# Performance work log

Hardware: AMD Instinct MI355X
Metric: run time of the kernel (lower is better)

Reference implementation:

```python
import jax, jax.numpy as jnp
import numpy as np

GROUP_SIZE = 64
OUT_F, IN_F = 4096, 4096


def _dequantize_3bit(packed_u8, params, group_size):
    # packed_u8: [num_groups * group_size//8*3] uint8; params: [num_groups, 2] (min, max)
    p = packed_u8.reshape(-1, 3)
    b0, b1, b2 = p[:, 0], p[:, 1], p[:, 2]
    q = jnp.stack([
        b0 & 7,
        (b0 >> 3) & 7,
        ((b0 >> 6) & 3) | ((b1 & 1) << 2),
        (b1 >> 1) & 7,
        (b1 >> 4) & 7,
        ((b1 >> 7) & 1) | ((b2 & 3) << 1),
        (b2 >> 2) & 7,
        (b2 >> 5) & 7,
    ], axis=-1)  # [N8, 8] uint8 in [0,7]
    num_groups = params.shape[0]
    q = q.reshape(num_groups, group_size).astype(jnp.float32)
    pf = params.astype(jnp.float32)
    x_min = pf[:, 0:1]
    scale = pf[:, 1:2] - x_min
    w = (q / 7.0) * scale + x_min
    return w.reshape(-1)


def setup_inputs() -> dict:
    key = jax.random.key(0)
    k1, k2, k3, k4 = jax.random.split(key, 4)
    num_groups = OUT_F * IN_F // GROUP_SIZE
    num_packed = num_groups * (GROUP_SIZE // 8 * 3)
    x = jax.random.normal(k1, (4, 2048, IN_F), dtype=jnp.float32)
    weight_q3 = jax.random.randint(k2, (num_packed,), 0, 256, dtype=jnp.int32)
    # realistic params: min < max per group
    raw = jax.random.normal(k3, (num_groups, 2), dtype=jnp.float32) * 0.02
    lo = jnp.minimum(raw[:, 0], raw[:, 1]) - 0.01
    hi = jnp.maximum(raw[:, 0], raw[:, 1]) + 0.01
    weight_params = jnp.stack([lo, hi], axis=-1).astype(jnp.float16)
    bias = jax.random.normal(k4, (OUT_F,), dtype=jnp.float32) * 0.02
    return {"x": x, "weight_q3": weight_q3, "weight_params": weight_params, "bias": bias}


def reference(x, weight_q3, weight_params, bias):
    packed = weight_q3.astype(jnp.uint8)
    w = _dequantize_3bit(packed, weight_params, GROUP_SIZE).reshape(OUT_F, IN_F)
    # F.linear: x @ W^T + b
    return jnp.einsum('bsi,oi->bso', x, w) + bias
```

## Files before the change

kernel.cpp:

```cpp
#include <hip/hip_runtime.h>
#include <hip/hip_fp16.h>
#include <stdint.h>

#define OUT_F 4096
#define IN_F  4096
#define M_DIM 8192
#define K_DIM IN_F
#define N_DIM OUT_F
#define GROUPS (OUT_F * IN_F / 64)
#define NTRIP  (GROUPS * 8)
#define NPARAM (GROUPS * 2)
#define NIT    (K_DIM / 128)

typedef __attribute__((ext_vector_type(4))) float f32x4;
typedef __attribute__((ext_vector_type(8))) short bf16x8;
typedef __attribute__((ext_vector_type(8))) unsigned short u16x8;

static __device__ __forceinline__ unsigned short f32_to_bf16(float f) {
    unsigned int u = __builtin_bit_cast(unsigned int, f);
    u += 0x7fffu + ((u >> 16) & 1u);
    return (unsigned short)(u >> 16);
}

__global__ void flag_init(int* f) { f[0] = 0; }

__global__ __launch_bounds__(256) void detect_f16(const __half* __restrict__ p,
                                                  int* __restrict__ flag) {
    int big = 0;
    for (int i = blockIdx.x * 256 + threadIdx.x; i < NPARAM; i += 256 * 256) {
        float v = __half2float(p[i]);
        if (!(fabsf(v) < 1.0f)) big = 1;
    }
    if (big) atomicOr(flag, 1);
}

__global__ __launch_bounds__(256) void dequant3(const int* __restrict__ pk,
                                                const void* __restrict__ params,
                                                const int* __restrict__ flag,
                                                unsigned short* __restrict__ W) {
    int t = blockIdx.x * 256 + threadIdx.x;
    int b0 = pk[3 * t + 0];
    int b1 = pk[3 * t + 1];
    int b2 = pk[3 * t + 2];
    int g = t >> 3;
    float lo, hi;
    if (flag[0] == 0) {
        const __half* p = (const __half*)params;
        lo = __half2float(p[2 * g + 0]);
        hi = __half2float(p[2 * g + 1]);
    } else {
        const float* p = (const float*)params;
        lo = p[2 * g + 0];
        hi = p[2 * g + 1];
    }
    float s = (hi - lo) * (1.0f / 7.0f);

    int q[8];
    q[0] = b0 & 7;
    q[1] = (b0 >> 3) & 7;
    q[2] = ((b0 >> 6) & 3) | ((b1 & 1) << 2);
    q[3] = (b1 >> 1) & 7;
    q[4] = (b1 >> 4) & 7;
    q[5] = ((b1 >> 7) & 1) | ((b2 & 3) << 1);
    q[6] = (b2 >> 2) & 7;
    q[7] = (b2 >> 5) & 7;

    u16x8 o;
#pragma unroll
    for (int j = 0; j < 8; j++) {
        float w = (float)q[j] * s + lo;
        o[j] = f32_to_bf16(w);
    }
    *(u16x8*)&W[8 * (size_t)t] = o;
}

__global__ __launch_bounds__(256) void cvt_x(const float* __restrict__ x,
                                             unsigned short* __restrict__ xb) {
    size_t t = (size_t)blockIdx.x * 256 + threadIdx.x;
    f32x4 a = *(const f32x4*)&x[8 * t];
    f32x4 b = *(const f32x4*)&x[8 * t + 4];
    u16x8 o;
#pragma unroll
    for (int j = 0; j < 4; j++) o[j] = f32_to_bf16(a[j]);
#pragma unroll
    for (int j = 0; j < 4; j++) o[4 + j] = f32_to_bf16(b[j]);
    *(u16x8*)&xb[8 * t] = o;
}


#define READ_AH(dst, b, h) do { _Pragma("unroll") for (int m2_ = 0; m2_ < 4; ++m2_) { \
    const char* p_ = shb + (b) * 49152 + arow_b + ((h) * 4 + m2_) * 2048; \
    dst[m2_][0] = *(const bf16x8*)(p_ + cb0); \
    dst[m2_][1] = *(const bf16x8*)(p_ + cb1); } } while (0)

#define READ_BT(dst, b) do { _Pragma("unroll") for (int n_ = 0; n_ < 2; ++n_) { \
    const char* p_ = shb + (b) * 49152 + 32768 + brow_b + n_ * 2048; \
    dst[n_][0] = *(const bf16x8*)(p_ + cb0); \
    dst[n_][1] = *(const bf16x8*)(p_ + cb1); } } while (0)

#define MFMA_H(h, As, Bs) do { __builtin_amdgcn_s_setprio(1); \
  _Pragma("unroll") for (int m2_ = 0; m2_ < 4; ++m2_) \
  _Pragma("unroll") for (int n_ = 0; n_ < 2; ++n_) { \
    acc[(h)*4+m2_][n_] = __builtin_amdgcn_mfma_f32_16x16x32_bf16(As[m2_][0], Bs[n_][0], acc[(h)*4+m2_][n_], 0,0,0); \
    acc[(h)*4+m2_][n_] = __builtin_amdgcn_mfma_f32_16x16x32_bf16(As[m2_][1], Bs[n_][1], acc[(h)*4+m2_][n_], 0,0,0); } \
  __builtin_amdgcn_s_setprio(0); } while (0)

#define STAGE_A(b, kt) do { _Pragma("unroll") for (int c_ = 0; c_ < 4; ++c_) { \
    const char* g_ = GAb + (size_t)(kt) * 128 + (size_t)(c_ * 64) * 8192; \
    unsigned short* l_ = &sh[(b) * 24576 + c_ * 4096 + w * 512]; \
    __builtin_amdgcn_global_load_lds((const __attribute__((address_space(1))) unsigned int*)(g_ + voff), \
        (__attribute__((address_space(3))) unsigned int*)l_, 16, 0, 0); } } while (0)

#define STAGE_B(b, kt) do { _Pragma("unroll") for (int c_ = 0; c_ < 2; ++c_) { \
    const char* g_ = GBb + (size_t)(kt) * 128 + (size_t)(c_ * 64) * 8192; \
    unsigned short* l_ = &sh[(b) * 24576 + 16384 + c_ * 4096 + w * 512]; \
    __builtin_amdgcn_global_load_lds((const __attribute__((address_space(1))) unsigned int*)(g_ + voff), \
        (__attribute__((address_space(3))) unsigned int*)l_, 16, 0, 0); } } while (0)

#define BAR() asm volatile("s_barrier" ::: "memory")
#define VMW(n) asm volatile("s_waitcnt vmcnt(" #n ")" ::: "memory")

__global__ __launch_bounds__(512, 1) void gemm4(const unsigned short* __restrict__ A,
                                                const unsigned short* __restrict__ B,
                                                const float* __restrict__ bias,
                                                float* __restrict__ C) {
    __shared__ unsigned short sh[2 * 24576];

    int bid = blockIdx.x;
    int swz = (bid & 7) * 128 + (bid >> 3);
    int bm = swz >> 5, bn = swz & 31;
    const int row0 = bm * 256, col0 = bn * 128;

    const int t = threadIdx.x;
    const int lane = t & 63;
    const int w = t >> 6;
    const int wm = w >> 2, wn = w & 3;

    const int l_hi = lane >> 3, l_lo = lane & 7;
    const int voff = (w * 8 + l_hi) * 8192 + ((l_lo ^ l_hi) * 16);

    const int fr = lane & 15;
    const int kg = lane >> 4;
    const int swzb = (lane & 7) << 4;
    const int cb0 = (kg * 16) ^ swzb;
    const int cb1 = (64 + kg * 16) ^ swzb;
    const int arow_b = (wm * 128 + fr) * 128;
    const int brow_b = (wn * 32 + fr) * 128;

    const char* GAb = (const char*)A + (size_t)row0 * 8192;
    const char* GBb = (const char*)B + (size_t)col0 * 8192;
    const char* shb = (const char*)sh;

    f32x4 acc[8][2] = {};
    bf16x8 Aa[4][2], Ab[4][2], Bx[2][2], By[2][2];

    STAGE_A(0, 0); STAGE_B(0, 0);
    STAGE_A(1, 1); STAGE_B(1, 1);
    VMW(6);
    BAR();
    READ_AH(Aa, 0, 0);
    READ_BT(Bx, 0);

    for (int it = 0; it < NIT; ++it) {
        const int ktx = 2 * it;
        const bool pf = (it + 1 < NIT);

        READ_AH(Ab, 0, 1);
        MFMA_H(0, Aa, Bx);
        VMW(0);
        BAR();
        READ_AH(Aa, 1, 0);
        READ_BT(By, 1);
        if (pf) { STAGE_A(0, ktx + 2); STAGE_B(0, ktx + 2); }
        MFMA_H(1, Ab, Bx);
        BAR();
        READ_AH(Ab, 1, 1);
        MFMA_H(0, Aa, By);
        VMW(0);
        BAR();
        if (pf) {
            READ_AH(Aa, 0, 0);
            READ_BT(Bx, 0);
            STAGE_A(1, ktx + 3); STAGE_B(1, ktx + 3);
        }
        MFMA_H(1, Ab, By);
        BAR();
    }

    const int crow = kg * 4;
    const int ccol = fr;
#pragma unroll
    for (int mi = 0; mi < 8; ++mi) {
#pragma unroll
        for (int ni = 0; ni < 2; ++ni) {
            int col = col0 + wn * 32 + ni * 16 + ccol;
            float bv = bias[col];
#pragma unroll
            for (int j = 0; j < 4; ++j) {
                int rw = row0 + wm * 128 + mi * 16 + crow + j;
                C[(size_t)rw * N_DIM + col] = acc[mi][ni][j] + bv;
            }
        }
    }
}

__global__ void ws_guard(float* out, float v) { out[0] = v; }

extern "C" void kernel_launch(void* const* d_in, const int* in_sizes, int n_in,
                              void* d_out, int out_size, void* d_ws, size_t ws_size,
                              hipStream_t stream) {
    const float* x      = (const float*)d_in[0];
    const int*   pk     = (const int*)d_in[1];
    const void*  params = (const void*)d_in[2];
    const float* bias   = (const float*)d_in[3];
    float* out = (float*)d_out;

    const size_t needW = (size_t)OUT_F * IN_F * 2;
    const size_t needX = (size_t)M_DIM * IN_F * 2;
    const size_t needF = 256;
    if (ws_size < needW + needX + needF) {
        ws_guard<<<1, 1, 0, stream>>>(out, 1.0e6f + (float)(ws_size >> 20));
        return;
    }
    unsigned short* W  = (unsigned short*)d_ws;
    unsigned short* Xb = (unsigned short*)((char*)d_ws + needW);
    int*            fl = (int*)((char*)d_ws + needW + needX);

    flag_init<<<1, 1, 0, stream>>>(fl);
    detect_f16<<<256, 256, 0, stream>>>((const __half*)params, fl);
    dequant3<<<NTRIP / 256, 256, 0, stream>>>(pk, params, fl, W);
    cvt_x<<<(int)(((size_t)M_DIM * IN_F / 8) / 256), 256, 0, stream>>>(x, Xb);
    gemm4<<<(M_DIM / 256) * (N_DIM / 128), 512, 0, stream>>>(Xb, W, bias, out);
}
```

Measured before the change: 326.5 us.

## Restructure GEMM to 4-wave blocks with triple-buffered 64-wide K stages

Replaces the 8-wave, double-buffered, K=128-per-stage GEMM with a 256-thread kernel that runs two blocks per CU. Each block keeps a 256x128 tile, with each wave computing 128x64. The K loop now advances 64 at a time through a three-slot LDS ring with rotating buffer offsets, and fragment reads are ping-ponged against MFMA issue. The LDS layout and XOR swizzle are reworked for 64-element rows. Each wave holds 32 accumulators, which risks register pressure under the 2-blocks occupancy bound, and the hand-unrolled tail must match the loop count exactly.

```diff
diff --git a/kernel.cpp b/kernel.cpp
--- a/kernel.cpp
+++ b/kernel.cpp
@@ -10,7 +10,6 @@
 #define GROUPS (OUT_F * IN_F / 64)
 #define NTRIP  (GROUPS * 8)
 #define NPARAM (GROUPS * 2)
-#define NIT    (K_DIM / 128)
 
 typedef __attribute__((ext_vector_type(4))) float f32x4;
 typedef __attribute__((ext_vector_type(8))) short bf16x8;
@@ -88,43 +87,39 @@
 }
 
 
-#define READ_AH(dst, b, h) do { _Pragma("unroll") for (int m2_ = 0; m2_ < 4; ++m2_) { \
-    const char* p_ = shb + (b) * 49152 + arow_b + ((h) * 4 + m2_) * 2048; \
-    dst[m2_][0] = *(const bf16x8*)(p_ + cb0); \
-    dst[m2_][1] = *(const bf16x8*)(p_ + cb1); } } while (0)
-
-#define READ_BT(dst, b) do { _Pragma("unroll") for (int n_ = 0; n_ < 2; ++n_) { \
-    const char* p_ = shb + (b) * 49152 + 32768 + brow_b + n_ * 2048; \
-    dst[n_][0] = *(const bf16x8*)(p_ + cb0); \
-    dst[n_][1] = *(const bf16x8*)(p_ + cb1); } } while (0)
-
-#define MFMA_H(h, As, Bs) do { __builtin_amdgcn_s_setprio(1); \
-  _Pragma("unroll") for (int m2_ = 0; m2_ < 4; ++m2_) \
-  _Pragma("unroll") for (int n_ = 0; n_ < 2; ++n_) { \
-    acc[(h)*4+m2_][n_] = __builtin_amdgcn_mfma_f32_16x16x32_bf16(As[m2_][0], Bs[n_][0], acc[(h)*4+m2_][n_], 0,0,0); \
-    acc[(h)*4+m2_][n_] = __builtin_amdgcn_mfma_f32_16x16x32_bf16(As[m2_][1], Bs[n_][1], acc[(h)*4+m2_][n_], 0,0,0); } \
+#define LGKM0 asm volatile("s_waitcnt lgkmcnt(0)" ::: "memory")
+#define VMW(n) asm volatile("s_waitcnt vmcnt(" #n ")" ::: "memory")
+#define BAR() asm volatile("s_barrier" ::: "memory")
+
+#define GLO(gp, lp) __builtin_amdgcn_global_load_lds( \
+    (const __attribute__((address_space(1))) unsigned int*)(gp), \
+    (__attribute__((address_space(3))) unsigned int*)(lp), 16, 0, 0)
+
+#define READ12(F, roff) do { \
+  _Pragma("unroll") for (int m_ = 0; m_ < 8; ++m_) \
+    F##A[m_] = *(const bf16x8*)(shb + (roff) + arow_b + m_ * 1024 + cbr); \
+  _Pragma("unroll") for (int n_ = 0; n_ < 4; ++n_) \
+    F##B[n_] = *(const bf16x8*)(shb + (roff) + 16384 + brow_b + n_ * 1024 + cbr); \
+} while (0)
+
+#define MFMA32(F) do { __builtin_amdgcn_s_setprio(1); \
+  _Pragma("unroll") for (int m_ = 0; m_ < 8; ++m_) \
+  _Pragma("unroll") for (int n_ = 0; n_ < 4; ++n_) \
+    acc[m_][n_] = __builtin_amdgcn_mfma_f32_16x16x32_bf16(F##A[m_], F##B[n_], acc[m_][n_], 0, 0, 0); \
   __builtin_amdgcn_s_setprio(0); } while (0)
 
-#define STAGE_A(b, kt) do { _Pragma("unroll") for (int c_ = 0; c_ < 4; ++c_) { \
-    const char* g_ = GAb + (size_t)(kt) * 128 + (size_t)(c_ * 64) * 8192; \
-    unsigned short* l_ = &sh[(b) * 24576 + c_ * 4096 + w * 512]; \
-    __builtin_amdgcn_global_load_lds((const __attribute__((address_space(1))) unsigned int*)(g_ + voff), \
-        (__attribute__((address_space(3))) unsigned int*)l_, 16, 0, 0); } } while (0)
-
-#define STAGE_B(b, kt) do { _Pragma("unroll") for (int c_ = 0; c_ < 2; ++c_) { \
-    const char* g_ = GBb + (size_t)(kt) * 128 + (size_t)(c_ * 64) * 8192; \
-    unsigned short* l_ = &sh[(b) * 24576 + 16384 + c_ * 4096 + w * 512]; \
-    __builtin_amdgcn_global_load_lds((const __attribute__((address_space(1))) unsigned int*)(g_ + voff), \
-        (__attribute__((address_space(3))) unsigned int*)l_, 16, 0, 0); } } while (0)
-
-#define BAR() asm volatile("s_barrier" ::: "memory")
-#define VMW(n) asm volatile("s_waitcnt vmcnt(" #n ")" ::: "memory")
-
-__global__ __launch_bounds__(512, 1) void gemm4(const unsigned short* __restrict__ A,
-                                                const unsigned short* __restrict__ B,
-                                                const float* __restrict__ bias,
-                                                float* __restrict__ C) {
-    __shared__ unsigned short sh[2 * 24576];
+#define STAGE(soff, kt) do { \
+  _Pragma("unroll") for (int c_ = 0; c_ < 4; ++c_) \
+    GLO(GAb + (size_t)(kt) * 64 + c_ * 524288 + vbase, shw + (soff) + c_ * 4096 + w4 * 1024); \
+  _Pragma("unroll") for (int c_ = 0; c_ < 2; ++c_) \
+    GLO(GBb + (size_t)(kt) * 64 + c_ * 524288 + vbase, shw + (soff) + 16384 + c_ * 4096 + w4 * 1024); \
+} while (0)
+
+__global__ __launch_bounds__(256, 2) void gemm_tb(const unsigned short* __restrict__ A,
+                                                  const unsigned short* __restrict__ B,
+                                                  const float* __restrict__ bias,
+                                                  float* __restrict__ C) {
+    __shared__ unsigned short sh[3 * 12288];
 
     int bid = blockIdx.x;
     int swz = (bid & 7) * 128 + (bid >> 3);
@@ -133,72 +128,70 @@
 
     const int t = threadIdx.x;
     const int lane = t & 63;
-    const int w = t >> 6;
-    const int wm = w >> 2, wn = w & 3;
-
-    const int l_hi = lane >> 3, l_lo = lane & 7;
-    const int voff = (w * 8 + l_hi) * 8192 + ((l_lo ^ l_hi) * 16);
+    const int w4 = t >> 6;
+    const int wm = w4 >> 1, wn = w4 & 1;
+
+    const int b2s = (lane >> 4) & 1;
+    const int lrow = ((lane >> 2) ^ b2s);
+    const int lchk = (lane & 3) ^ (lrow & 3);
+    const int vbase = (w4 * 16 + lrow) * 8192 + lchk * 16;
 
     const int fr = lane & 15;
     const int kg = lane >> 4;
-    const int swzb = (lane & 7) << 4;
-    const int cb0 = (kg * 16) ^ swzb;
-    const int cb1 = (64 + kg * 16) ^ swzb;
-    const int arow_b = (wm * 128 + fr) * 128;
-    const int brow_b = (wn * 32 + fr) * 128;
+    const int b2f = (fr >> 2) & 1;
+    const int cbr = ((kg ^ (fr & 3)) << 4);
+    const int arow_b = (wm * 128 + (fr ^ b2f)) * 64;
+    const int brow_b = (wn * 64 + (fr ^ b2f)) * 64;
 
     const char* GAb = (const char*)A + (size_t)row0 * 8192;
     const char* GBb = (const char*)B + (size_t)col0 * 8192;
     const char* shb = (const char*)sh;
-
-    f32x4 acc[8][2] = {};
-    bf16x8 Aa[4][2], Ab[4][2], Bx[2][2], By[2][2];
-
-    STAGE_A(0, 0); STAGE_B(0, 0);
-    STAGE_A(1, 1); STAGE_B(1, 1);
+    char* shw = (char*)sh;
+
+    f32x4 acc[8][4] = {};
+    bf16x8 FaA[8], FaB[4], FbA[8], FbB[4];
+
+    STAGE(0, 0); STAGE(24576, 1); STAGE(49152, 2);
     VMW(6);
     BAR();
-    READ_AH(Aa, 0, 0);
-    READ_BT(Bx, 0);
-
-    for (int it = 0; it < NIT; ++it) {
-        const int ktx = 2 * it;
-        const bool pf = (it + 1 < NIT);
-
-        READ_AH(Ab, 0, 1);
-        MFMA_H(0, Aa, Bx);
-        VMW(0);
-        BAR();
-        READ_AH(Aa, 1, 0);
-        READ_BT(By, 1);
-        if (pf) { STAGE_A(0, ktx + 2); STAGE_B(0, ktx + 2); }
-        MFMA_H(1, Ab, Bx);
-        BAR();
-        READ_AH(Ab, 1, 1);
-        MFMA_H(0, Aa, By);
-        VMW(0);
-        BAR();
-        if (pf) {
-            READ_AH(Aa, 0, 0);
-            READ_BT(Bx, 0);
-            STAGE_A(1, ktx + 3); STAGE_B(1, ktx + 3);
-        }
-        MFMA_H(1, Ab, By);
-        BAR();
-    }
+    READ12(Fa, 0);
+    LGKM0;
+    BAR();
+
+    int r0 = 0, r1 = 24576, r2 = 49152;
+
+    for (int j = 0; j < 61; ++j) {
+        const int kb = 2 * j;
+        READ12(Fb, r1);
+        STAGE(r0, kb + 3);
+        MFMA32(Fa);
+        LGKM0; VMW(6); BAR();
+        READ12(Fa, r2);
+        STAGE(r1, kb + 4);
+        MFMA32(Fb);
+        LGKM0; VMW(6); BAR();
+        int tmp = r0; r0 = r2; r2 = r1; r1 = tmp;
+    }
+    READ12(Fb, r1); STAGE(r0, 125); MFMA32(Fa); LGKM0; VMW(6); BAR();
+    READ12(Fa, r2); STAGE(r1, 126); MFMA32(Fb); LGKM0; VMW(6); BAR();
+    { int tmp = r0; r0 = r2; r2 = r1; r1 = tmp; }
+    READ12(Fb, r1); STAGE(r0, 127); MFMA32(Fa); LGKM0; VMW(6); BAR();
+    READ12(Fa, r2);                 MFMA32(Fb); LGKM0; VMW(0); BAR();
+    READ12(Fb, r0);                 MFMA32(Fa); LGKM0; BAR();
+    MFMA32(Fb);
 
     const int crow = kg * 4;
     const int ccol = fr;
 #pragma unroll
     for (int mi = 0; mi < 8; ++mi) {
 #pragma unroll
-        for (int ni = 0; ni < 2; ++ni) {
-            int col = col0 + wn * 32 + ni * 16 + ccol;
+        for (int ni = 0; ni < 4; ++ni) {
+            int col = col0 + wn * 64 + ni * 16 + ccol;
             float bv = bias[col];
 #pragma unroll
-            for (int j = 0; j < 4; ++j) {
-                int rw = row0 + wm * 128 + mi * 16 + crow + j;
-                C[(size_t)rw * N_DIM + col] = acc[mi][ni][j] + bv;
+            for (int jj = 0; jj < 4; ++jj) {
+                int rw = row0 + wm * 128 + mi * 16 + crow + jj;
+                C[(size_t)rw * N_DIM + col] = acc[mi][ni][jj] + bv;
             }
         }
     }
@@ -230,5 +223,5 @@
     detect_f16<<<256, 256, 0, stream>>>((const __half*)params, fl);
     dequant3<<<NTRIP / 256, 256, 0, stream>>>(pk, params, fl, W);
     cvt_x<<<(int)(((size_t)M_DIM * IN_F / 8) / 256), 256, 0, stream>>>(x, Xb);
-    gemm4<<<(M_DIM / 256) * (N_DIM / 128), 512, 0, stream>>>(Xb, W, bias, out);
-}
+    gemm_tb<<<(M_DIM / 256) * (N_DIM / 128), 256, 0, stream>>>(Xb, W, bias, out);
+}
```

After: 329.6 us. Within noise of the previous version (+1.0%).
